# Kernel tuning notes

Measured on AMD Instinct MI355X. Metric: run time of the kernel, lower is better.

Reference implementation:

```python
import jax, jax.numpy as jnp
import numpy as np

B, S, D = 4, 8192, 512
H, DK = 8, 64
LOCAL_W = 256
GLOBAL_STRIDE = 64
LN_EPS = 1e-5


def setup_inputs() -> dict:
    key = jax.random.key(0)
    ks = jax.random.split(key, 9)
    scale = 1.0 / np.sqrt(D)
    def lin(k, din, dout):
        return jax.random.normal(k, (din, dout), jnp.float32) * scale
    return {
        "x": jax.random.normal(ks[0], (B, S, D), jnp.float32),
        "lq_w": lin(ks[1], D, D), "lq_b": jnp.zeros((D,), jnp.float32),
        "lk_w": lin(ks[2], D, D), "lk_b": jnp.zeros((D,), jnp.float32),
        "lv_w": lin(ks[3], D, D), "lv_b": jnp.zeros((D,), jnp.float32),
        "gq_w": lin(ks[4], D, D), "gq_b": jnp.zeros((D,), jnp.float32),
        "gk_w": lin(ks[5], D, D), "gk_b": jnp.zeros((D,), jnp.float32),
        "gv_w": lin(ks[6], D, D), "gv_b": jnp.zeros((D,), jnp.float32),
        "out_w": jax.random.normal(ks[7], (2 * D, D), jnp.float32) * (1.0 / np.sqrt(2 * D)),
        "out_b": jnp.zeros((D,), jnp.float32),
        "ln_g": jnp.ones((D,), jnp.float32),
        "ln_b": jnp.zeros((D,), jnp.float32),
    }


def _local_attention(x, qw, qb, kw, kb, vw, vb):
    # x: [B,S,D]; S divisible by LOCAL_W -> no padding path.
    nW = S // LOCAL_W
    xw = x.reshape(B, nW, LOCAL_W, D)
    def heads(w, b):
        y = jnp.einsum('bnwd,de->bnwe', xw, w) + b  # [B,nW,W,D]
        return y.reshape(B, nW, LOCAL_W, H, DK).transpose(0, 1, 3, 2, 4)  # [B,nW,H,W,dk]
    q, k, v = heads(qw, qb), heads(kw, kb), heads(vw, vb)
    scores = jnp.einsum('bnhqd,bnhkd->bnhqk', q, k) / np.sqrt(DK)
    attn = jax.nn.softmax(scores, axis=-1)
    out = jnp.einsum('bnhqk,bnhkd->bnhqd', attn, v)  # [B,nW,H,W,dk]
    return out.transpose(0, 1, 3, 2, 4).reshape(B, S, D)


def _global_attention(x, qw, qb, kw, kb, vw, vb):
    gc = x[:, ::GLOBAL_STRIDE]                       # [B,G,D]
    G = gc.shape[1]
    q = (x @ qw + qb).reshape(B, S, H, DK)           # [B,S,H,dk]
    k = (gc @ kw + kb).reshape(B, G, H, DK)
    v = (gc @ vw + vb).reshape(B, G, H, DK)
    scores = jnp.einsum('bshd,bghd->bhsg', q, k) / np.sqrt(DK)
    attn = jax.nn.softmax(scores, axis=-1)
    out = jnp.einsum('bhsg,bghd->bshd', attn, v)
    return out.reshape(B, S, D)


def reference(x, lq_w, lq_b, lk_w, lk_b, lv_w, lv_b,
              gq_w, gq_b, gk_w, gk_b, gv_w, gv_b,
              out_w, out_b, ln_g, ln_b):
    local = _local_attention(x, lq_w, lq_b, lk_w, lk_b, lv_w, lv_b)
    glob = _global_attention(x, gq_w, gq_b, gk_w, gk_b, gv_w, gv_b)
    combined = jnp.concatenate([local, glob], axis=-1) @ out_w + out_b
    h = x + combined  # dropout is identity in eval
    mu = jnp.mean(h, axis=-1, keepdims=True)
    var = jnp.var(h, axis=-1, keepdims=True)
    return (h - mu) / jnp.sqrt(var + LN_EPS) * ln_g + ln_b
```

## Files before the change

### kernel.cpp

```cpp
#include <hip/hip_runtime.h>
#include <hip/hip_bf16.h>
#include <stdint.h>

#define B_ 4
#define S_ 8192
#define D_ 512
#define H_ 8
#define DK_ 64
#define G_ 128
#define ROWS_ (B_*S_)

typedef unsigned short u16;
typedef __attribute__((ext_vector_type(8))) short short8;
typedef __attribute__((ext_vector_type(4))) short short4v;
typedef __attribute__((ext_vector_type(4))) float floatx4;

static __device__ __forceinline__ float bf2f(u16 u){
  union { uint32_t i; float f; } v; v.i = ((uint32_t)u) << 16; return v.f;
}
static __device__ __forceinline__ u16 f2bf(float f){
  union { float f; uint32_t i; } v; v.f = f;
  uint32_t u = v.i; u += 0x7fff + ((u >> 16) & 1); return (u16)(u >> 16);
}

static __device__ __forceinline__ void glds16(const u16* g, u16* l){
  __builtin_amdgcn_global_load_lds(
      (const __attribute__((address_space(1))) void*)g,
      (__attribute__((address_space(3))) void*)l, 16, 0, 0);
}

__global__ void cast_x_kernel(const float* __restrict__ x, u16* __restrict__ xb, int n4){
  int i = blockIdx.x*blockDim.x + threadIdx.x;
  if (i >= n4) return;
  float4 v = ((const float4*)x)[i];
  short4v o;
  o[0] = (short)f2bf(v.x); o[1] = (short)f2bf(v.y);
  o[2] = (short)f2bf(v.z); o[3] = (short)f2bf(v.w);
  *(short4v*)(xb + (size_t)i*4) = o;
}

__global__ void transpose_cast_kernel(const float* __restrict__ W, u16* __restrict__ Ot, int K, int N){
  __shared__ float t[64][65];
  int n0 = blockIdx.x*64, k0 = blockIdx.y*64;
  int tx = threadIdx.x & 63, ty = threadIdx.x >> 6;
#pragma unroll
  for (int j=0;j<16;j++){ int k = ty + j*4; t[k][tx] = W[(size_t)(k0+k)*N + n0+tx]; }
  __syncthreads();
#pragma unroll
  for (int j=0;j<16;j++){ int n = ty + j*4; Ot[(size_t)(n0+n)*K + k0 + tx] = f2bf(t[tx][n]); }
}

__global__ void build_bias_kernel(float* __restrict__ bcat, float* __restrict__ bg,
    const float* lq_b, const float* lk_b, const float* lv_b, const float* gq_b,
    const float* gk_b, const float* gv_b){
  int i = blockIdx.x*blockDim.x + threadIdx.x;
  if (i < 2048){
    const float* s = (i < 512) ? lq_b : (i < 1024) ? lk_b : (i < 1536) ? lv_b : gq_b;
    bcat[i] = s[i & 511];
  } else if (i < 3072){
    int j = i - 2048;
    bg[j] = (j < 512) ? gk_b[j] : gv_b[j - 512];
  }
}

__global__ void gather_xg_kernel(const u16* __restrict__ xb, u16* __restrict__ xg){
  int t = blockIdx.x*blockDim.x + threadIdx.x;
  int row = t >> 6;
  int c8 = (t & 63) * 8;
  int b = row >> 7, g = row & 127;
  const u16* src = xb + ((size_t)(b*S_ + g*64))*D_ + c8;
  u16* dst = xg + (size_t)row*D_ + c8;
  *(short8*)dst = *(const short8*)src;
}

template<int EPI>
__global__ __launch_bounds__(512, 1) void gemm_big(
    const u16* __restrict__ A, const u16* __restrict__ Bt,
    const float* __restrict__ bias, u16* __restrict__ C,
    const u16* __restrict__ X, int M, int N, int K)
{
  __shared__ u16 SM[4][16384];
  const int tid = threadIdx.x, lane = tid & 63, w = tid >> 6;
  const int wm = w >> 2, wn = w & 3;
  const int gx = gridDim.x;
  const int h = blockIdx.y * gx + blockIdx.x;
  const int chunk = (gx * gridDim.y) >> 3;
  const int work = (h & 7) * chunk + (h >> 3);
  const int bx = work % gx, by = work / gx;
  const int m0 = by*256, n0 = bx*256;
  const int T = K >> 5;

  const u16* gsrc[4]; int loff[4];
#pragma unroll
  for (int j = 0; j < 4; j++){
    int fb  = w*4 + j;
    int isB = fb >> 4;
    int blk = fb & 15;
    const u16* bp = isB ? Bt : A;
    int row = (isB ? n0 : m0) + blk*16 + (lane & 15);
    gsrc[j] = bp + (size_t)row * K + ((lane >> 4) * 8);
    loff[j] = fb*512;
  }

  floatx4 acc[8][4] = {};

#pragma unroll
  for (int tt = 0; tt < 3; tt++)
#pragma unroll
    for (int j = 0; j < 4; j++)
      glds16(gsrc[j] + tt*32, &SM[tt][loff[j]]);

#pragma unroll 4
  for (int t = 0; t < T; t++){
    if (t <= T - 3)      asm volatile("s_waitcnt vmcnt(8)" ::: "memory");
    else if (t == T - 2) asm volatile("s_waitcnt vmcnt(4)" ::: "memory");
    else                 asm volatile("s_waitcnt vmcnt(0)" ::: "memory");
    __builtin_amdgcn_s_barrier();

    if (t + 3 < T){
      u16* Sb = &SM[(t + 3) & 3][0];
#pragma unroll
      for (int j = 0; j < 4; j++) glds16(gsrc[j] + (t+3)*32, Sb + loff[j]);
    }

    const u16* Tb = &SM[t & 3][0];
    short8 aR[8], bR[4];
#pragma unroll
    for (int i=0;i<8;i++) aR[i] = *(const short8*)(Tb + (wm*8 + i)*512 + lane*8);
#pragma unroll
    for (int j=0;j<4;j++) bR[j] = *(const short8*)(Tb + (16 + wn*4 + j)*512 + lane*8);
#pragma unroll
    for (int i=0;i<8;i++)
#pragma unroll
      for (int j=0;j<4;j++)
        acc[i][j] = __builtin_amdgcn_mfma_f32_16x16x32_bf16(aR[i], bR[j], acc[i][j], 0,0,0);
  }

#pragma unroll
  for (int mi=0; mi<8; mi++)
#pragma unroll
    for (int nj=0; nj<4; nj++){
      int col = n0 + (wn*4 + nj)*16 + (lane & 15);
      float bv = bias[col];
#pragma unroll
      for (int ii=0; ii<4; ii++){
        size_t row = (size_t)(m0 + (wm*8 + mi)*16 + (lane>>4)*4 + ii);
        float v = acc[mi][nj][ii] + bv;
        if (EPI == 1) v += bf2f(X[row*N + col]);
        C[row*N + col] = f2bf(v);
      }
    }
}

__global__ __launch_bounds__(256) void gemm_small(
    const u16* __restrict__ A, const u16* __restrict__ Bt,
    const float* __restrict__ bias, u16* __restrict__ C,
    int M, int N, int K)
{
  __shared__ u16 As[128*32];
  __shared__ u16 Bs[128*32];
  const int tid = threadIdx.x, lane = tid & 63, w = tid >> 6;
  const int m0 = blockIdx.y*128, n0 = blockIdx.x*128;
  const int wm = (w>>1)*64, wn = (w&1)*64;
  floatx4 acc[4][4] = {};
  const int c0 = 2*w;
  const int sr = lane >> 2;
  const int sc = (lane & 3) * 8;
  const u16* ga0 = A  + (size_t)(m0 +  c0     *16 + sr)*K + sc;
  const u16* ga1 = A  + (size_t)(m0 + (c0 + 1)*16 + sr)*K + sc;
  const u16* gb0 = Bt + (size_t)(n0 +  c0     *16 + sr)*K + sc;
  const u16* gb1 = Bt + (size_t)(n0 + (c0 + 1)*16 + sr)*K + sc;
  u16* la0 = &As[ c0     *512];
  u16* la1 = &As[(c0 + 1)*512];
  u16* lb0 = &Bs[ c0     *512];
  u16* lb1 = &Bs[(c0 + 1)*512];

  for (int k0 = 0; k0 < K; k0 += 32){
    __syncthreads();
    glds16(ga0 + k0, la0);
    glds16(ga1 + k0, la1);
    glds16(gb0 + k0, lb0);
    glds16(gb1 + k0, lb1);
    __syncthreads();
    short8 af[4], bf[4];
#pragma unroll
    for (int i=0;i<4;i++) af[i] = *(const short8*)&As[(wm + i*16 + (lane&15))*32 + (lane>>4)*8];
#pragma unroll
    for (int i=0;i<4;i++) bf[i] = *(const short8*)&Bs[(wn + i*16 + (lane&15))*32 + (lane>>4)*8];
#pragma unroll
    for (int mi=0;mi<4;mi++)
#pragma unroll
      for (int ni=0;ni<4;ni++)
        acc[mi][ni] = __builtin_amdgcn_mfma_f32_16x16x32_bf16(af[mi], bf[ni], acc[mi][ni], 0,0,0);
  }

#pragma unroll
  for (int mi=0;mi<4;mi++)
#pragma unroll
    for (int ni=0;ni<4;ni++){
      int col = n0 + wn + ni*16 + (lane&15);
      float bv = bias[col];
#pragma unroll
      for (int i=0;i<4;i++){
        size_t row = (size_t)(m0 + wm + mi*16 + (lane>>4)*4 + i);
        C[row*N + col] = f2bf(acc[mi][ni][i] + bv);
      }
    }
}

template<int KVLEN, int KSTRIDE, bool GLOBAL>
__global__ __launch_bounds__(512, 2) void attn_kernel(
    const u16* __restrict__ qkv, const u16* __restrict__ kvbuf, u16* __restrict__ comb)
{
  __shared__ u16 SM[KVLEN*256];
  u16* Kl = SM;
  u16* Vt = SM + KVLEN*64;
  u16* Pl = SM + KVLEN*128;
  const int tid = threadIdx.x, lane = tid & 63, w = tid >> 6;
  const int h = blockIdx.x, n = blockIdx.y, b = blockIdx.z;
  const size_t qrow0 = (size_t)b*S_ + (size_t)n*256;
  const int krow0 = GLOBAL ? b*G_ : (b*S_ + n*256);
  const int qc = (GLOBAL ? 1536 : 0)   + h*DK_;
  const int kc = (GLOBAL ? 0    : 512) + h*DK_;
  const int vc = (GLOBAL ? 512  : 1024)+ h*DK_;
  const int oc = (GLOBAL ? 512  : 0)   + h*DK_;
  constexpr int NF = KVLEN/16;

  {
    const int rpw = KVLEN/8;
    const int r0w = w * rpw;
    const int cg = ((lane & 7) ^ (lane >> 3)) * 8;
    const int rl = lane >> 3;
#pragma unroll
    for (int j = 0; j < rpw; j += 8){
      int row = r0w + j + rl;
      glds16(kvbuf + (size_t)(krow0 + row)*KSTRIDE + kc + cg, &Kl[(r0w + j)*64]);
    }
  }
  if (tid < KVLEN){
    const int r0 = (tid >> 3) * 8;
    const int c0 = (tid & 7) * 8;
    const u16* vp = kvbuf + (size_t)(krow0 + r0)*KSTRIDE + vc + c0;
    short8 rIn[8];
#pragma unroll
    for (int i=0;i<8;i++) rIn[i] = *(const short8*)(vp + (size_t)i*KSTRIDE);
#pragma unroll
    for (int i=0;i<8;i++){
      short8 o;
#pragma unroll
      for (int j=0;j<8;j++) o[j] = rIn[j][i];
      int d = c0 + i;
      *(short8*)&Vt[d*KVLEN + ((((r0>>3) ^ (d&7))) << 3)] = o;
    }
  }
  __syncthreads();

  const float scale = 0.125f;
  const int Pbase = w*16*KVLEN;

  for (int sp = 2*w; sp < 2*w + 2; sp++){
    const u16* qp = qkv + (qrow0 + sp*16 + (lane&15))*2048 + qc + ((lane>>4)*8);
    short8 qf0 = *(const short8*)qp;
    short8 qf1 = *(const short8*)(qp + 32);

    floatx4 sacc[NF];
#pragma unroll
    for (int nf = 0; nf < NF; nf++){
      const u16* kb = &Kl[(nf*16 + (lane&15))*64];
      short8 kf0 = *(const short8*)(kb + ((( lane>>4)      ^ (lane&7)) << 3));
      short8 kf1 = *(const short8*)(kb + ((((lane>>4) + 4) ^ (lane&7)) << 3));
      floatx4 z = {0.f,0.f,0.f,0.f};
      z = __builtin_amdgcn_mfma_f32_16x16x32_bf16(qf0, kf0, z, 0,0,0);
      z = __builtin_amdgcn_mfma_f32_16x16x32_bf16(qf1, kf1, z, 0,0,0);
      sacc[nf] = z;
    }

    float mx[4] = {-1e30f,-1e30f,-1e30f,-1e30f};
#pragma unroll
    for (int nf=0;nf<NF;nf++)
#pragma unroll
      for (int i=0;i<4;i++) mx[i] = fmaxf(mx[i], sacc[nf][i]);
#pragma unroll
    for (int i=0;i<4;i++){
#pragma unroll
      for (int msk=1; msk<16; msk<<=1) mx[i] = fmaxf(mx[i], __shfl_xor(mx[i], msk));
    }
    float sm[4] = {0.f,0.f,0.f,0.f};
#pragma unroll
    for (int nf=0;nf<NF;nf++)
#pragma unroll
      for (int i=0;i<4;i++){
        float e = __expf((sacc[nf][i] - mx[i]) * scale);
        sacc[nf][i] = e; sm[i] += e;
      }
#pragma unroll
    for (int i=0;i<4;i++){
#pragma unroll
      for (int msk=1; msk<16; msk<<=1) sm[i] += __shfl_xor(sm[i], msk);
      sm[i] = 1.f / sm[i];
    }

#pragma unroll
    for (int nf=0;nf<NF;nf++)
#pragma unroll
      for (int i=0;i<4;i++){
        int row = (lane>>4)*4 + i;
        int ch  = nf*2 + ((lane>>3)&1);
        Pl[Pbase + row*KVLEN + ((ch ^ (row&7)) << 3) + (lane&7)] = f2bf(sacc[nf][i]*sm[i]);
      }

    floatx4 oacc[4] = {};
#pragma unroll
    for (int kk=0; kk<KVLEN/32; kk++){
      int prow = lane & 15;
      short8 pf = *(const short8*)&Pl[Pbase + prow*KVLEN + (((kk*4 + (lane>>4)) ^ (prow&7)) << 3)];
#pragma unroll
      for (int nd=0; nd<4; nd++){
        int d = nd*16 + (lane&15);
        short8 vf = *(const short8*)&Vt[d*KVLEN + (((kk*4 + (lane>>4)) ^ (d&7)) << 3)];
        oacc[nd] = __builtin_amdgcn_mfma_f32_16x16x32_bf16(pf, vf, oacc[nd], 0,0,0);
      }
    }

#pragma unroll
    for (int nd=0; nd<4; nd++)
#pragma unroll
      for (int i=0;i<4;i++){
        size_t row = qrow0 + sp*16 + (lane>>4)*4 + i;
        comb[row*1024 + oc + nd*16 + (lane&15)] = f2bf(oacc[nd][i]);
      }
  }
}

__global__ __launch_bounds__(256) void ln_kernel(const u16* __restrict__ hb,
    float* __restrict__ out, const float* __restrict__ g, const float* __restrict__ bta){
  int lane = threadIdx.x & 63, w = threadIdx.x >> 6;
  size_t row = (size_t)blockIdx.x*4 + w;
  const u16* p = hb + row*D_;
  short8 hv = *(const short8*)(p + lane*8);
  float f[8]; float s = 0.f, q = 0.f;
#pragma unroll
  for (int i=0;i<8;i++){ f[i] = bf2f((u16)hv[i]); s += f[i]; q += f[i]*f[i]; }
#pragma unroll
  for (int msk=1; msk<64; msk<<=1){ s += __shfl_xor(s, msk); q += __shfl_xor(q, msk); }
  float mean = s * (1.f/512.f);
  float var  = q * (1.f/512.f) - mean*mean;
  float inv  = rsqrtf(var + 1e-5f);
  float4 g0 = ((const float4*)g)[lane*2],   g1 = ((const float4*)g)[lane*2+1];
  float4 b0 = ((const float4*)bta)[lane*2], b1 = ((const float4*)bta)[lane*2+1];
  float4 o0, o1;
  o0.x = (f[0]-mean)*inv*g0.x + b0.x; o0.y = (f[1]-mean)*inv*g0.y + b0.y;
  o0.z = (f[2]-mean)*inv*g0.z + b0.z; o0.w = (f[3]-mean)*inv*g0.w + b0.w;
  o1.x = (f[4]-mean)*inv*g1.x + b1.x; o1.y = (f[5]-mean)*inv*g1.y + b1.y;
  o1.z = (f[6]-mean)*inv*g1.z + b1.z; o1.w = (f[7]-mean)*inv*g1.w + b1.w;
  float* op = out + row*D_;
  ((float4*)op)[lane*2]     = o0;
  ((float4*)op)[lane*2 + 1] = o1;
}

extern "C" void kernel_launch(void* const* d_in, const int* in_sizes, int n_in,
                              void* d_out, int out_size, void* d_ws, size_t ws_size,
                              hipStream_t stream)
{
  const float* x    = (const float*)d_in[0];
  const float* lq_w = (const float*)d_in[1];
  const float* lq_b = (const float*)d_in[2];
  const float* lk_w = (const float*)d_in[3];
  const float* lk_b = (const float*)d_in[4];
  const float* lv_w = (const float*)d_in[5];
  const float* lv_b = (const float*)d_in[6];
  const float* gq_w = (const float*)d_in[7];
  const float* gq_b = (const float*)d_in[8];
  const float* gk_w = (const float*)d_in[9];
  const float* gk_b = (const float*)d_in[10];
  const float* gv_w = (const float*)d_in[11];
  const float* gv_b = (const float*)d_in[12];
  const float* out_w = (const float*)d_in[13];
  const float* out_b = (const float*)d_in[14];
  const float* ln_g = (const float*)d_in[15];
  const float* ln_b = (const float*)d_in[16];

  char* ws = (char*)d_ws;
  size_t off = 0;
  auto alloc = [&](size_t bytes)->void*{ void* p = ws + off; off += (bytes + 255) & ~255ULL; return p; };
  u16*  xb    = (u16*) alloc((size_t)ROWS_*D_*2);
  u16*  xg    = (u16*) alloc((size_t)512*512*2);
  u16*  WcatT = (u16*) alloc((size_t)2048*512*2);
  u16*  WgT   = (u16*) alloc((size_t)1024*512*2);
  u16*  WoutT = (u16*) alloc((size_t)512*1024*2);
  float* bcat = (float*)alloc(2048*4);
  float* bg   = (float*)alloc(1024*4);
  u16*  qkvg  = (u16*) alloc((size_t)ROWS_*2048*2);
  u16*  gkv   = (u16*) alloc((size_t)512*1024*2);
  u16*  comb  = (u16*) alloc((size_t)ROWS_*1024*2);
  u16*  hbuf  = qkvg;

  cast_x_kernel<<<16384,256,0,stream>>>(x, xb, ROWS_*D_/4);
  transpose_cast_kernel<<<dim3(8,8),256,0,stream>>>(lq_w, WcatT + (size_t)0*512*512, 512, 512);
  transpose_cast_kernel<<<dim3(8,8),256,0,stream>>>(lk_w, WcatT + (size_t)1*512*512, 512, 512);
  transpose_cast_kernel<<<dim3(8,8),256,0,stream>>>(lv_w, WcatT + (size_t)2*512*512, 512, 512);
  transpose_cast_kernel<<<dim3(8,8),256,0,stream>>>(gq_w, WcatT + (size_t)3*512*512, 512, 512);
  transpose_cast_kernel<<<dim3(8,8),256,0,stream>>>(gk_w, WgT, 512, 512);
  transpose_cast_kernel<<<dim3(8,8),256,0,stream>>>(gv_w, WgT + (size_t)512*512, 512, 512);
  transpose_cast_kernel<<<dim3(8,16),256,0,stream>>>(out_w, WoutT, 1024, 512);
  build_bias_kernel<<<12,256,0,stream>>>(bcat, bg, lq_b, lk_b, lv_b, gq_b, gk_b, gv_b);
  gather_xg_kernel<<<128,256,0,stream>>>(xb, xg);

  gemm_big<0><<<dim3(8,128),512,0,stream>>>(xb, WcatT, bcat, qkvg, nullptr, ROWS_, 2048, 512);
  gemm_small<<<dim3(8,4),256,0,stream>>>(xg, WgT, bg, gkv, 512, 1024, 512);

  attn_kernel<256,2048,false><<<dim3(8,32,4),512,0,stream>>>(qkvg, qkvg, comb);
  attn_kernel<128,1024,true ><<<dim3(8,32,4),512,0,stream>>>(qkvg, gkv,  comb);

  gemm_big<1><<<dim3(2,128),512,0,stream>>>(comb, WoutT, out_b, hbuf, xb, ROWS_, 512, 1024);
  ln_kernel<<<8192,256,0,stream>>>(hbuf, (float*)d_out, ln_g, ln_b);
}
```

Measured before the change: 293.0 us.

## Fuse output projection with residual and LayerNorm, merge prep kernels

The output GEMM is replaced by a new gemm_ln kernel. Each block computes full 128x512 rows, adds bias and residual, and applies LayerNorm using a cross-wave reduction in shared memory. This removes the bf16 intermediate buffer and the separate LN pass. The xg gather is folded into the x cast kernel, the six weight transposes become one launch, and the V transpose in attention now uses 4-row chunks with more threads. The risks are fewer blocks (256) for the last GEMM, a new 3-stage pipeline, and more register pressure.

```diff
diff --git a/kernel.cpp b/kernel.cpp
--- a/kernel.cpp
+++ b/kernel.cpp
@@ -29,7 +29,8 @@
       (__attribute__((address_space(3))) void*)l, 16, 0, 0);
 }
 
-__global__ void cast_x_kernel(const float* __restrict__ x, u16* __restrict__ xb, int n4){
+__global__ void cast_x_kernel(const float* __restrict__ x, u16* __restrict__ xb,
+                              u16* __restrict__ xg, int n4){
   int i = blockIdx.x*blockDim.x + threadIdx.x;
   if (i >= n4) return;
   float4 v = ((const float4*)x)[i];
@@ -37,6 +38,11 @@
   o[0] = (short)f2bf(v.x); o[1] = (short)f2bf(v.y);
   o[2] = (short)f2bf(v.z); o[3] = (short)f2bf(v.w);
   *(short4v*)(xb + (size_t)i*4) = o;
+  int row = i >> 7;
+  if ((row & 63) == 0){
+    int b = row >> 13, g = (row & 8191) >> 6;
+    *(short4v*)(xg + ((size_t)(b*G_ + g)*D_) + (i & 127)*4) = o;
+  }
 }
 
 __global__ void transpose_cast_kernel(const float* __restrict__ W, u16* __restrict__ Ot, int K, int N){
@@ -48,6 +54,22 @@
   __syncthreads();
 #pragma unroll
   for (int j=0;j<16;j++){ int n = ty + j*4; Ot[(size_t)(n0+n)*K + k0 + tx] = f2bf(t[tx][n]); }
+}
+
+__global__ void transpose_cast6_kernel(const float* s0, const float* s1, const float* s2,
+    const float* s3, const float* s4, const float* s5,
+    u16* __restrict__ WcatT, u16* __restrict__ WgT){
+  __shared__ float t[64][65];
+  int z = blockIdx.z;
+  const float* W = (z==0)?s0:(z==1)?s1:(z==2)?s2:(z==3)?s3:(z==4)?s4:s5;
+  u16* Ot = (z<4) ? (WcatT + (size_t)z*512*512) : (WgT + (size_t)(z-4)*512*512);
+  int n0 = blockIdx.x*64, k0 = blockIdx.y*64;
+  int tx = threadIdx.x & 63, ty = threadIdx.x >> 6;
+#pragma unroll
+  for (int j=0;j<16;j++){ int k = ty + j*4; t[k][tx] = W[(size_t)(k0+k)*512 + n0+tx]; }
+  __syncthreads();
+#pragma unroll
+  for (int j=0;j<16;j++){ int n = ty + j*4; Ot[(size_t)(n0+n)*512 + k0 + tx] = f2bf(t[tx][n]); }
 }
 
 __global__ void build_bias_kernel(float* __restrict__ bcat, float* __restrict__ bg,
@@ -63,21 +85,10 @@
   }
 }
 
-__global__ void gather_xg_kernel(const u16* __restrict__ xb, u16* __restrict__ xg){
-  int t = blockIdx.x*blockDim.x + threadIdx.x;
-  int row = t >> 6;
-  int c8 = (t & 63) * 8;
-  int b = row >> 7, g = row & 127;
-  const u16* src = xb + ((size_t)(b*S_ + g*64))*D_ + c8;
-  u16* dst = xg + (size_t)row*D_ + c8;
-  *(short8*)dst = *(const short8*)src;
-}
-
-template<int EPI>
 __global__ __launch_bounds__(512, 1) void gemm_big(
     const u16* __restrict__ A, const u16* __restrict__ Bt,
     const float* __restrict__ bias, u16* __restrict__ C,
-    const u16* __restrict__ X, int M, int N, int K)
+    int M, int N, int K)
 {
   __shared__ u16 SM[4][16384];
   const int tid = threadIdx.x, lane = tid & 63, w = tid >> 6;
@@ -145,9 +156,130 @@
 #pragma unroll
       for (int ii=0; ii<4; ii++){
         size_t row = (size_t)(m0 + (wm*8 + mi)*16 + (lane>>4)*4 + ii);
-        float v = acc[mi][nj][ii] + bv;
-        if (EPI == 1) v += bf2f(X[row*N + col]);
-        C[row*N + col] = f2bf(v);
+        C[row*N + col] = f2bf(acc[mi][nj][ii] + bv);
+      }
+    }
+}
+
+__global__ __launch_bounds__(512, 1) void gemm_ln(
+    const u16* __restrict__ A, const u16* __restrict__ Bt,
+    const float* __restrict__ bias, const u16* __restrict__ X,
+    const float* __restrict__ lng, const float* __restrict__ lnb,
+    float* __restrict__ out)
+{
+  constexpr int K = 1024, N = 512;
+  constexpr int T = K >> 5;
+  __shared__ u16 SM[3][20480];
+  __shared__ float red[128][4][2];
+  const int tid = threadIdx.x, lane = tid & 63, w = tid >> 6;
+  const int wm = w >> 2, wn = w & 3;
+  const int h = blockIdx.y;
+  const int work = (h & 7) * 32 + (h >> 3);
+  const int m0 = work * 128;
+
+  const u16* gsrc[5]; int loff[5];
+#pragma unroll
+  for (int j = 0; j < 5; j++){
+    int fb = w*5 + j;
+    int isB = (fb >= 8);
+    int blk = isB ? (fb - 8) : fb;
+    const u16* bp = isB ? Bt : A;
+    int row = (isB ? 0 : m0) + blk*16 + (lane & 15);
+    gsrc[j] = bp + (size_t)row * K + ((lane >> 4) * 8);
+    loff[j] = fb*512;
+  }
+
+  floatx4 acc[4][8] = {};
+
+#pragma unroll
+  for (int tt = 0; tt < 2; tt++)
+#pragma unroll
+    for (int j = 0; j < 5; j++)
+      glds16(gsrc[j] + tt*32, &SM[tt][loff[j]]);
+
+  for (int t = 0; t < T; t++){
+    if (t + 1 < T) asm volatile("s_waitcnt vmcnt(5)" ::: "memory");
+    else           asm volatile("s_waitcnt vmcnt(0)" ::: "memory");
+    __builtin_amdgcn_s_barrier();
+
+    if (t + 2 < T){
+      u16* Sb = &SM[(t + 2) % 3][0];
+#pragma unroll
+      for (int j = 0; j < 5; j++) glds16(gsrc[j] + (t+2)*32, Sb + loff[j]);
+    }
+
+    const u16* Tb = &SM[t % 3][0];
+    short8 aR[4], bR[8];
+#pragma unroll
+    for (int i=0;i<4;i++) aR[i] = *(const short8*)(Tb + (wm*4 + i)*512 + lane*8);
+#pragma unroll
+    for (int j=0;j<8;j++) bR[j] = *(const short8*)(Tb + (8 + wn*8 + j)*512 + lane*8);
+#pragma unroll
+    for (int i=0;i<4;i++)
+#pragma unroll
+      for (int j=0;j<8;j++)
+        acc[i][j] = __builtin_amdgcn_mfma_f32_16x16x32_bf16(aR[i], bR[j], acc[i][j], 0,0,0);
+  }
+
+  float bv[8], gv[8], bb[8];
+#pragma unroll
+  for (int nj=0;nj<8;nj++){
+    int col = wn*128 + nj*16 + (lane & 15);
+    bv[nj] = bias[col]; gv[nj] = lng[col]; bb[nj] = lnb[col];
+  }
+  float sv[4][4], qv[4][4];
+#pragma unroll
+  for (int mi=0;mi<4;mi++)
+#pragma unroll
+    for (int ii=0;ii<4;ii++){ sv[mi][ii]=0.f; qv[mi][ii]=0.f; }
+#pragma unroll
+  for (int mi=0;mi<4;mi++)
+#pragma unroll
+    for (int nj=0;nj<8;nj++){
+      int col = wn*128 + nj*16 + (lane & 15);
+#pragma unroll
+      for (int ii=0;ii<4;ii++){
+        size_t row = (size_t)(m0 + wm*64 + mi*16 + (lane>>4)*4 + ii);
+        float v = acc[mi][nj][ii] + bv[nj] + bf2f(X[row*N + col]);
+        acc[mi][nj][ii] = v;
+        sv[mi][ii] += v; qv[mi][ii] += v*v;
+      }
+    }
+#pragma unroll
+  for (int mi=0;mi<4;mi++)
+#pragma unroll
+    for (int ii=0;ii<4;ii++)
+#pragma unroll
+      for (int msk=1; msk<16; msk<<=1){
+        sv[mi][ii] += __shfl_xor(sv[mi][ii], msk);
+        qv[mi][ii] += __shfl_xor(qv[mi][ii], msk);
+      }
+  if ((lane & 15) == 0){
+#pragma unroll
+    for (int mi=0;mi<4;mi++)
+#pragma unroll
+      for (int ii=0;ii<4;ii++){
+        int rl = wm*64 + mi*16 + (lane>>4)*4 + ii;
+        red[rl][wn][0] = sv[mi][ii];
+        red[rl][wn][1] = qv[mi][ii];
+      }
+  }
+  __syncthreads();
+#pragma unroll
+  for (int mi=0;mi<4;mi++)
+#pragma unroll
+    for (int ii=0;ii<4;ii++){
+      int rl = wm*64 + mi*16 + (lane>>4)*4 + ii;
+      float ss = red[rl][0][0] + red[rl][1][0] + red[rl][2][0] + red[rl][3][0];
+      float qq = red[rl][0][1] + red[rl][1][1] + red[rl][2][1] + red[rl][3][1];
+      float mean = ss * (1.f/512.f);
+      float var  = qq * (1.f/512.f) - mean*mean;
+      float inv  = rsqrtf(var + 1e-5f);
+      size_t row = (size_t)(m0 + rl);
+#pragma unroll
+      for (int nj=0;nj<8;nj++){
+        int col = wn*128 + nj*16 + (lane & 15);
+        out[row*N + col] = (acc[mi][nj][ii] - mean)*inv*gv[nj] + bb[nj];
       }
     }
 }
@@ -237,20 +369,23 @@
       glds16(kvbuf + (size_t)(krow0 + row)*KSTRIDE + kc + cg, &Kl[(r0w + j)*64]);
     }
   }
-  if (tid < KVLEN){
-    const int r0 = (tid >> 3) * 8;
-    const int c0 = (tid & 7) * 8;
-    const u16* vp = kvbuf + (size_t)(krow0 + r0)*KSTRIDE + vc + c0;
-    short8 rIn[8];
-#pragma unroll
-    for (int i=0;i<8;i++) rIn[i] = *(const short8*)(vp + (size_t)i*KSTRIDE);
-#pragma unroll
-    for (int i=0;i<8;i++){
-      short8 o;
-#pragma unroll
-      for (int j=0;j<8;j++) o[j] = rIn[j][i];
-      int d = c0 + i;
-      *(short8*)&Vt[d*KVLEN + ((((r0>>3) ^ (d&7))) << 3)] = o;
+  if (tid < (KVLEN/4)*8){
+    const int rb = tid >> 3;
+    const int kv0 = rb * 4;
+    const int d0 = (tid & 7) * 8;
+    const u16* vp = kvbuf + (size_t)(krow0 + kv0)*KSTRIDE + vc + d0;
+    short8 rIn[4];
+#pragma unroll
+    for (int i=0;i<4;i++) rIn[i] = *(const short8*)(vp + (size_t)i*KSTRIDE);
+    const int c   = rb >> 1;
+    const int sub = kv0 & 7;
+#pragma unroll
+    for (int dd=0; dd<8; dd++){
+      int d = d0 + dd;
+      short4v o;
+#pragma unroll
+      for (int j=0;j<4;j++) o[j] = rIn[j][dd];
+      *(short4v*)&Vt[d*KVLEN + ((c ^ (d&7)) << 3) + sub] = o;
     }
   }
   __syncthreads();
@@ -330,32 +465,6 @@
         comb[row*1024 + oc + nd*16 + (lane&15)] = f2bf(oacc[nd][i]);
       }
   }
-}
-
-__global__ __launch_bounds__(256) void ln_kernel(const u16* __restrict__ hb,
-    float* __restrict__ out, const float* __restrict__ g, const float* __restrict__ bta){
-  int lane = threadIdx.x & 63, w = threadIdx.x >> 6;
-  size_t row = (size_t)blockIdx.x*4 + w;
-  const u16* p = hb + row*D_;
-  short8 hv = *(const short8*)(p + lane*8);
-  float f[8]; float s = 0.f, q = 0.f;
-#pragma unroll
-  for (int i=0;i<8;i++){ f[i] = bf2f((u16)hv[i]); s += f[i]; q += f[i]*f[i]; }
-#pragma unroll
-  for (int msk=1; msk<64; msk<<=1){ s += __shfl_xor(s, msk); q += __shfl_xor(q, msk); }
-  float mean = s * (1.f/512.f);
-  float var  = q * (1.f/512.f) - mean*mean;
-  float inv  = rsqrtf(var + 1e-5f);
-  float4 g0 = ((const float4*)g)[lane*2],   g1 = ((const float4*)g)[lane*2+1];
-  float4 b0 = ((const float4*)bta)[lane*2], b1 = ((const float4*)bta)[lane*2+1];
-  float4 o0, o1;
-  o0.x = (f[0]-mean)*inv*g0.x + b0.x; o0.y = (f[1]-mean)*inv*g0.y + b0.y;
-  o0.z = (f[2]-mean)*inv*g0.z + b0.z; o0.w = (f[3]-mean)*inv*g0.w + b0.w;
-  o1.x = (f[4]-mean)*inv*g1.x + b1.x; o1.y = (f[5]-mean)*inv*g1.y + b1.y;
-  o1.z = (f[6]-mean)*inv*g1.z + b1.z; o1.w = (f[7]-mean)*inv*g1.w + b1.w;
-  float* op = out + row*D_;
-  ((float4*)op)[lane*2]     = o0;
-  ((float4*)op)[lane*2 + 1] = o1;
 }
 
 extern "C" void kernel_launch(void* const* d_in, const int* in_sizes, int n_in,
@@ -393,25 +502,17 @@
   u16*  qkvg  = (u16*) alloc((size_t)ROWS_*2048*2);
   u16*  gkv   = (u16*) alloc((size_t)512*1024*2);
   u16*  comb  = (u16*) alloc((size_t)ROWS_*1024*2);
-  u16*  hbuf  = qkvg;
-
-  cast_x_kernel<<<16384,256,0,stream>>>(x, xb, ROWS_*D_/4);
-  transpose_cast_kernel<<<dim3(8,8),256,0,stream>>>(lq_w, WcatT + (size_t)0*512*512, 512, 512);
-  transpose_cast_kernel<<<dim3(8,8),256,0,stream>>>(lk_w, WcatT + (size_t)1*512*512, 512, 512);
-  transpose_cast_kernel<<<dim3(8,8),256,0,stream>>>(lv_w, WcatT + (size_t)2*512*512, 512, 512);
-  transpose_cast_kernel<<<dim3(8,8),256,0,stream>>>(gq_w, WcatT + (size_t)3*512*512, 512, 512);
-  transpose_cast_kernel<<<dim3(8,8),256,0,stream>>>(gk_w, WgT, 512, 512);
-  transpose_cast_kernel<<<dim3(8,8),256,0,stream>>>(gv_w, WgT + (size_t)512*512, 512, 512);
+
+  cast_x_kernel<<<16384,256,0,stream>>>(x, xb, xg, ROWS_*D_/4);
+  transpose_cast6_kernel<<<dim3(8,8,6),256,0,stream>>>(lq_w, lk_w, lv_w, gq_w, gk_w, gv_w, WcatT, WgT);
   transpose_cast_kernel<<<dim3(8,16),256,0,stream>>>(out_w, WoutT, 1024, 512);
   build_bias_kernel<<<12,256,0,stream>>>(bcat, bg, lq_b, lk_b, lv_b, gq_b, gk_b, gv_b);
-  gather_xg_kernel<<<128,256,0,stream>>>(xb, xg);
-
-  gemm_big<0><<<dim3(8,128),512,0,stream>>>(xb, WcatT, bcat, qkvg, nullptr, ROWS_, 2048, 512);
+
+  gemm_big<<<dim3(8,128),512,0,stream>>>(xb, WcatT, bcat, qkvg, ROWS_, 2048, 512);
   gemm_small<<<dim3(8,4),256,0,stream>>>(xg, WgT, bg, gkv, 512, 1024, 512);
 
   attn_kernel<256,2048,false><<<dim3(8,32,4),512,0,stream>>>(qkvg, qkvg, comb);
   attn_kernel<128,1024,true ><<<dim3(8,32,4),512,0,stream>>>(qkvg, gkv,  comb);
 
-  gemm_big<1><<<dim3(2,128),512,0,stream>>>(comb, WoutT, out_b, hbuf, xb, ROWS_, 512, 1024);
-  ln_kernel<<<8192,256,0,stream>>>(hbuf, (float*)d_out, ln_g, ln_b);
-}
+  gemm_ln<<<dim3(1,256),512,0,stream>>>(comb, WoutT, out_b, xb, ln_g, ln_b, (float*)d_out);
+}
```

Result: slower. 305.5 us (+4.3%).
